# Optimization experiments

Hardware: AMD Instinct MI355X
Metric: run time of the kernel (lower is better)

## Reference

```python
import jax, jax.numpy as jnp
import numpy as np

N = 40000          # nodes
E = 640000         # edges
D_IN, D_HID, D_EMB, D_OUT = 128, 128, 64, 2


def glorot(key, shape):
    lim = np.sqrt(6.0 / (shape[0] + shape[1]))
    return jax.random.uniform(key, shape, jnp.float32, -lim, lim)


def setup_inputs() -> dict:
    key = jax.random.key(0)
    ks = jax.random.split(key, 8)
    x = jax.random.normal(ks[0], (N, D_IN), jnp.float32)
    edge_index = jax.random.randint(ks[1], (2, E), 0, N, dtype=jnp.int64)
    # GCNConv weights stored as [in, out]; biases zero-init per PyG default
    W1 = glorot(ks[2], (D_IN, D_HID));  b1 = jnp.zeros((D_HID,), jnp.float32)
    W2 = glorot(ks[3], (D_HID, D_HID)); b2 = jnp.zeros((D_HID,), jnp.float32)
    W3 = glorot(ks[4], (D_HID, D_EMB)); b3 = jnp.zeros((D_EMB,), jnp.float32)
    Wout = glorot(ks[5], (D_EMB, D_OUT)); bout = jnp.zeros((D_OUT,), jnp.float32)
    return {"x": x, "edge_index": edge_index,
            "W1": W1, "b1": b1, "W2": W2, "b2": b2,
            "W3": W3, "b3": b3, "Wout": Wout, "bout": bout}


def _gcn_norm(edge_index, n):
    # add self loops, compute symmetric normalization d^-1/2[src] * d^-1/2[dst]
    loop = jnp.arange(n, dtype=edge_index.dtype)
    src = jnp.concatenate([edge_index[0], loop])
    dst = jnp.concatenate([edge_index[1], loop])
    deg = jax.ops.segment_sum(jnp.ones_like(dst, dtype=jnp.float32), dst,
                              num_segments=n)
    dinv = jax.lax.rsqrt(deg)                      # deg >= 1 due to self-loops
    dinv = jnp.where(jnp.isinf(dinv), 0.0, dinv)
    return src, dst, dinv[src] * dinv[dst]


def gcn_conv(x, src, dst, norm, W, b):
    h = x @ W                                      # [N, out]
    msg = h[src] * norm[:, None]                   # gather + scale  [E+N, out]
    return jax.ops.segment_sum(msg, dst, num_segments=x.shape[0]) + b


def reference(x, edge_index, W1, b1, W2, b2, W3, b3, Wout, bout):
    n = x.shape[0]
    src, dst, norm = _gcn_norm(edge_index, n)      # cached=True: computed once
    h = jax.nn.relu(gcn_conv(x, src, dst, norm, W1, b1))   # dropout is identity in eval
    h = jax.nn.relu(gcn_conv(h, src, dst, norm, W2, b2))
    h = gcn_conv(h, src, dst, norm, W3, b3)
    out = h @ Wout + bout
    return (out, h)
```

## Files before the change

kernel.cpp:

```cpp
#include <hip/hip_runtime.h>
#include <hip/hip_bf16.h>

#define NN 40000
#define NE 640000

typedef unsigned int u32;
typedef unsigned short u16;
typedef __attribute__((ext_vector_type(8))) short bf16x8;
typedef __attribute__((ext_vector_type(4))) float f32x4;

__device__ float g_wf[512];
__device__ u16   g_wp[40960];
__device__ int   g_flags[4];
__device__ int   g_cnt[NN];
__device__ int   g_cur[NN];
__device__ int   g_rowptr[NN + 1];
__device__ float g_dinv[NN];
__device__ int   g_csrc[NE];
__device__ int   g_bsum[64];
__device__ u16   g_ha[(size_t)NN * 128];
__device__ u16   g_hb[(size_t)NN * 128];

#define OFF_B1 0
#define OFF_B2 128
#define OFF_B3 256
#define OFF_WO 320
#define OFF_BO 448
#define WP_W1 0
#define WP_W2 16384
#define WP_W3 32768

__device__ __forceinline__ float b2f(u16 v){ return __uint_as_float(((u32)v) << 16); }
__device__ __forceinline__ float blo(u32 u){ return __uint_as_float(u << 16); }
__device__ __forceinline__ float bhi(u32 u){ return __uint_as_float(u & 0xffff0000u); }
__device__ __forceinline__ u32 f2bf(float f){
  u32 u = __float_as_uint(f);
  return (u + 0x7fffu + ((u >> 16) & 1u)) >> 16;
}
__device__ __forceinline__ int clampi(int v, int lo, int hi){ return v < lo ? lo : (v > hi ? hi : v); }
__device__ __forceinline__ u16 ldbf(const void* p, int idx){
  return g_flags[0] ? (u16)f2bf(((const float*)p)[idx]) : ((const u16*)p)[idx];
}
__device__ __forceinline__ float ldf(const void* p, int idx){
  return g_flags[0] ? ((const float*)p)[idx] : b2f(((const u16*)p)[idx]);
}

__global__ __launch_bounds__(256) void k_detect(const u16* __restrict__ xf, const int* __restrict__ ei){
  __shared__ int c1, c2;
  if (threadIdx.x == 0){ c1 = 0; c2 = 0; }
  __syncthreads();
  int l1 = 0, l2 = 0;
  for (int i = threadIdx.x; i < 4096; i += 256){
    u16 v = xf[2 * i];
    int e = (v >> 7) & 0xff;
    if (v == 0 || (e >= 100 && e <= 140)) l1++;
    if (ei[2 * i + 1] == 0) l2++;
  }
  atomicAdd(&c1, l1); atomicAdd(&c2, l2);
  __syncthreads();
  if (threadIdx.x == 0){
    g_flags[0] = (c1 < 2048) ? 1 : 0;
    g_flags[1] = (c2 > 2048) ? 2 : 1;
  }
}

__global__ __launch_bounds__(256) void k_prep(const void* xin, const void* w1, const void* b1,
                                              const void* w2, const void* b2, const void* w3,
                                              const void* b3, const void* wo, const void* bo){
  int T = (int)blockIdx.x * 256 + (int)threadIdx.x;
  if (T < 640000){
    if (g_flags[0]){
      const float4* p = (const float4*)xin + (size_t)T * 2;
      float4 a = p[0], b = p[1];
      uint4 o;
      o.x = f2bf(a.x) | (f2bf(a.y) << 16);
      o.y = f2bf(a.z) | (f2bf(a.w) << 16);
      o.z = f2bf(b.x) | (f2bf(b.y) << 16);
      o.w = f2bf(b.z) | (f2bf(b.w) << 16);
      ((uint4*)g_ha)[T] = o;
    } else {
      ((uint4*)g_ha)[T] = ((const uint4*)xin)[T];
    }
  } else if (T < 680960){
    int local = T - 640000;
    int J, dstbase, l; const void* src;
    if (local < 16384){ J = 128; src = w1; dstbase = WP_W1; l = local; }
    else if (local < 32768){ J = 128; src = w2; dstbase = WP_W2; l = local - 16384; }
    else { J = 64; src = w3; dstbase = WP_W3; l = local - 32768; }
    int chunk = l >> 9, within = l & 511;
    int nbw = J / 16;
    int kb = chunk / nbw, nb = chunk % nbw;
    int lane = within >> 3, j = within & 7;
    int q = lane >> 4, n = lane & 15;
    int k = kb * 32 + q * 8 + j;
    int col = nb * 16 + n;
    g_wp[dstbase + l] = ldbf(src, k * J + col);
  } else if (T < 681410){
    int l = T - 680960;
    if (l < 128)      g_wf[OFF_B1 + l] = ldf(b1, l);
    else if (l < 256) g_wf[OFF_B2 + l - 128] = ldf(b2, l - 128);
    else if (l < 320) g_wf[OFF_B3 + l - 256] = ldf(b3, l - 256);
    else if (l < 448) g_wf[OFF_WO + l - 320] = ldf(wo, l - 320);
    else              g_wf[OFF_BO + l - 448] = ldf(bo, l - 448);
  } else if (T < 721410){
    g_cnt[T - 681410] = 0;
  } else if (T < 761450){
    g_cur[T - 721410] = 0;
  }
}

__global__ __launch_bounds__(256) void k_count(const int* __restrict__ ei){
  int e = blockIdx.x * 256 + threadIdx.x;
  if (e < NE){
    int strd = g_flags[1];
    int d = clampi(ei[(size_t)(NE + e) * strd], 0, NN - 1);
    atomicAdd(&g_cnt[d], 1);
  }
}

__global__ __launch_bounds__(1024) void k_scan1(){
  int t = (int)threadIdx.x;
  int b = (int)blockIdx.x;
  int i = b * 1024 + t;
  int v = (i < NN) ? g_cnt[i] : 0;
  int lane = t & 63, wv = t >> 6;
  int x = v;
#pragma unroll
  for (int ofs = 1; ofs < 64; ofs <<= 1){
    int y = __shfl_up(x, ofs, 64);
    if (lane >= ofs) x += y;
  }
  __shared__ int wsum[16];
  if (lane == 63) wsum[wv] = x;
  __syncthreads();
  if (t < 16){
    int s = wsum[t];
#pragma unroll
    for (int ofs = 1; ofs < 16; ofs <<= 1){
      int y = __shfl_up(s, ofs, 64);
      if (t >= ofs) s += y;
    }
    wsum[t] = s;
  }
  __syncthreads();
  int pre = (wv == 0) ? 0 : wsum[wv - 1];
  int incl = x + pre;
  if (i < NN){
    g_rowptr[i] = incl - v;
    g_dinv[i] = rsqrtf((float)(v + 1));
  }
  if (t == 1023) g_bsum[b] = incl;
}

__global__ __launch_bounds__(1024) void k_scan3(){
  __shared__ int pre;
  int t = (int)threadIdx.x;
  if (t < 64){
    int v = (t < 40) ? g_bsum[t] : 0;
    int s = v;
#pragma unroll
    for (int ofs = 1; ofs < 64; ofs <<= 1){
      int y = __shfl_up(s, ofs, 64);
      if (t >= ofs) s += y;
    }
    if (t == (int)blockIdx.x) pre = s - v;
    if (blockIdx.x == 0 && t == 39) g_rowptr[NN] = s;
  }
  __syncthreads();
  int i = (int)blockIdx.x * 1024 + t;
  if (i < NN) g_rowptr[i] += pre;
}

__global__ __launch_bounds__(256) void k_fill(const int* __restrict__ ei){
  int part = (int)blockIdx.x & 7;
  int chunk = (int)blockIdx.x >> 3;
  int lo = part * 5000, hi = lo + 5000;
  int strd = g_flags[1];
  int tid = (int)threadIdx.x;
#pragma unroll
  for (int it = 0; it < 8; ++it){
    int e = chunk * 2048 + it * 256 + tid;
    if (e < NE){
      int d = clampi(ei[(size_t)(NE + e) * strd], 0, NN - 1);
      if (d >= lo && d < hi){
        int s = clampi(ei[(size_t)e * strd], 0, NN - 1);
        int pos = clampi(g_rowptr[d] + atomicAdd(&g_cur[d], 1), 0, NE - 1);
        g_csrc[pos] = s;
      }
    }
  }
}

template<int J>
__global__ __launch_bounds__(256) void k_gemm(int wpoff){
  constexpr int NB = J / 16;
  int tid = (int)threadIdx.x;
  int wave = tid >> 6, lane = tid & 63;
  int q = lane >> 4, n = lane & 15;
  int m0 = (int)blockIdx.x * 64 + wave * 16;
  f32x4 acc[NB];
#pragma unroll
  for (int nb = 0; nb < NB; ++nb) acc[nb] = (f32x4){0.f, 0.f, 0.f, 0.f};
  const u16* arow = g_ha + (size_t)(m0 + n) * 128 + q * 8;
#pragma unroll
  for (int kb = 0; kb < 4; ++kb){
    bf16x8 a = *(const bf16x8*)(arow + kb * 32);
    const u16* wbase = g_wp + wpoff + (kb * NB) * 512 + lane * 8;
#pragma unroll
    for (int nb = 0; nb < NB; ++nb){
      bf16x8 w = *(const bf16x8*)(wbase + nb * 512);
      acc[nb] = __builtin_amdgcn_mfma_f32_16x16x32_bf16(a, w, acc[nb], 0, 0, 0);
    }
  }
  u16* crow = g_hb + (size_t)(m0 + q * 4) * J + n;
#pragma unroll
  for (int r = 0; r < 4; ++r){
    float di = g_dinv[m0 + q * 4 + r];
#pragma unroll
    for (int nb = 0; nb < NB; ++nb)
      crow[(size_t)r * J + nb * 16] = (u16)f2bf(acc[nb][r] * di);
  }
}

template<int J, bool RELU>
__global__ __launch_bounds__(256) void k_agg(int boff, float* __restrict__ h3, float* __restrict__ outp){
  int wpair = (int)((blockIdx.x * 256 + threadIdx.x) >> 6);
  int lane = (int)threadIdx.x & 63;
  int sub = lane >> 5, sl = lane & 31;
  int wid = wpair * 2 + sub;
  if (wid >= NN) return;
  float di = g_dinv[wid];
  int beg = g_rowptr[wid], end = g_rowptr[wid + 1];
  if (J == 128){
    int cc = sl * 4;
    float a0 = 0.f, a1 = 0.f, a2 = 0.f, a3 = 0.f;
    int e = beg;
    for (; e + 7 < end; e += 8){
      int s[8]; uint2 p[8];
#pragma unroll
      for (int t = 0; t < 8; ++t) s[t] = clampi(g_csrc[e + t], 0, NN - 1);
#pragma unroll
      for (int t = 0; t < 8; ++t) p[t] = *(const uint2*)(g_hb + (size_t)s[t] * 128 + cc);
#pragma unroll
      for (int t = 0; t < 8; ++t){
        a0 += blo(p[t].x); a1 += bhi(p[t].x);
        a2 += blo(p[t].y); a3 += bhi(p[t].y);
      }
    }
    for (; e < end; ++e){
      int s0 = clampi(g_csrc[e], 0, NN - 1);
      uint2 p0 = *(const uint2*)(g_hb + (size_t)s0 * 128 + cc);
      a0 += blo(p0.x); a1 += bhi(p0.x);
      a2 += blo(p0.y); a3 += bhi(p0.y);
    }
    uint2 ps = *(const uint2*)(g_hb + (size_t)wid * 128 + cc);
    a0 += blo(ps.x); a1 += bhi(ps.x);
    a2 += blo(ps.y); a3 += bhi(ps.y);
    a0 = a0 * di + g_wf[boff + cc];
    a1 = a1 * di + g_wf[boff + cc + 1];
    a2 = a2 * di + g_wf[boff + cc + 2];
    a3 = a3 * di + g_wf[boff + cc + 3];
    if (RELU){
      a0 = fmaxf(a0, 0.f); a1 = fmaxf(a1, 0.f);
      a2 = fmaxf(a2, 0.f); a3 = fmaxf(a3, 0.f);
    }
    uint2 o;
    o.x = f2bf(a0) | (f2bf(a1) << 16);
    o.y = f2bf(a2) | (f2bf(a3) << 16);
    *(uint2*)(g_ha + (size_t)wid * 128 + cc) = o;
  } else {
    int cc = sl * 2;
    float a0 = 0.f, a1 = 0.f;
    int e = beg;
    for (; e + 7 < end; e += 8){
      int s[8]; u32 p[8];
#pragma unroll
      for (int t = 0; t < 8; ++t) s[t] = clampi(g_csrc[e + t], 0, NN - 1);
#pragma unroll
      for (int t = 0; t < 8; ++t) p[t] = *(const u32*)(g_hb + (size_t)s[t] * 64 + cc);
#pragma unroll
      for (int t = 0; t < 8; ++t){ a0 += blo(p[t]); a1 += bhi(p[t]); }
    }
    for (; e < end; ++e){
      int s0 = clampi(g_csrc[e], 0, NN - 1);
      u32 p0 = *(const u32*)(g_hb + (size_t)s0 * 64 + cc);
      a0 += blo(p0); a1 += bhi(p0);
    }
    u32 ps = *(const u32*)(g_hb + (size_t)wid * 64 + cc);
    a0 += blo(ps); a1 += bhi(ps);
    a0 = a0 * di + g_wf[boff + cc];
    a1 = a1 * di + g_wf[boff + cc + 1];
    if (RELU){ a0 = fmaxf(a0, 0.f); a1 = fmaxf(a1, 0.f); }
    *(float2*)(h3 + (size_t)wid * 64 + cc) = make_float2(a0, a1);
    float o0 = a0 * g_wf[OFF_WO + cc * 2]     + a1 * g_wf[OFF_WO + cc * 2 + 2];
    float o1 = a0 * g_wf[OFF_WO + cc * 2 + 1] + a1 * g_wf[OFF_WO + cc * 2 + 3];
#pragma unroll
    for (int m = 1; m < 32; m <<= 1){
      o0 += __shfl_xor(o0, m, 64);
      o1 += __shfl_xor(o1, m, 64);
    }
    if (sl == 0){
      *(float2*)(outp + (size_t)wid * 2) =
        make_float2(o0 + g_wf[OFF_BO], o1 + g_wf[OFF_BO + 1]);
    }
  }
}

extern "C" void kernel_launch(void* const* d_in, const int* in_sizes, int n_in,
                              void* d_out, int out_size, void* d_ws, size_t ws_size,
                              hipStream_t stream){
  const int* ei = (const int*)d_in[1];
  float* out = (float*)d_out;
  float* h3  = out + (size_t)NN * 2;

  k_detect<<<1, 256, 0, stream>>>((const u16*)d_in[0], ei);
  k_prep<<<2975, 256, 0, stream>>>(d_in[0], d_in[2], d_in[3], d_in[4], d_in[5],
                                   d_in[6], d_in[7], d_in[8], d_in[9]);
  k_count<<<2500, 256, 0, stream>>>(ei);
  k_scan1<<<40, 1024, 0, stream>>>();
  k_scan3<<<40, 1024, 0, stream>>>();
  k_fill<<<2504, 256, 0, stream>>>(ei);

  k_gemm<128><<<625, 256, 0, stream>>>(WP_W1);
  k_agg<128, true><<<5000, 256, 0, stream>>>(OFF_B1, (float*)nullptr, (float*)nullptr);
  k_gemm<128><<<625, 256, 0, stream>>>(WP_W2);
  k_agg<128, true><<<5000, 256, 0, stream>>>(OFF_B2, (float*)nullptr, (float*)nullptr);
  k_gemm<64><<<625, 256, 0, stream>>>(WP_W3);
  k_agg<64, false><<<5000, 256, 0, stream>>>(OFF_B3, h3, out);
}
```

Measured before the change: 259.9 us.

## Compact edge indices to 16-bit and simplify CSR fill to one pass

The count kernel now also writes source and destination indices as 16-bit values into compact arrays. The fill kernel reads these instead of re-scanning the strided int64 edge list with an 8-way partitioned pass, and writes a 16-bit CSR column array. The aggregation kernels then read half the index bytes and skip the clamps. Node ids below 65536 fit in u16, but the fill loses its partition-by-destination locality, which may increase atomic contention.

```diff
diff --git a/kernel.cpp b/kernel.cpp
--- a/kernel.cpp
+++ b/kernel.cpp
@@ -16,7 +16,9 @@
 __device__ int   g_cur[NN];
 __device__ int   g_rowptr[NN + 1];
 __device__ float g_dinv[NN];
-__device__ int   g_csrc[NE];
+__device__ u16   g_es[NE];
+__device__ u16   g_ed[NE];
+__device__ u16   g_csrc16[NE];
 __device__ int   g_bsum[64];
 __device__ u16   g_ha[(size_t)NN * 128];
 __device__ u16   g_hb[(size_t)NN * 128];
@@ -113,7 +115,10 @@
   int e = blockIdx.x * 256 + threadIdx.x;
   if (e < NE){
     int strd = g_flags[1];
+    int s = clampi(ei[(size_t)e * strd], 0, NN - 1);
     int d = clampi(ei[(size_t)(NE + e) * strd], 0, NN - 1);
+    g_es[e] = (u16)s;
+    g_ed[e] = (u16)d;
     atomicAdd(&g_cnt[d], 1);
   }
 }
@@ -171,23 +176,12 @@
   if (i < NN) g_rowptr[i] += pre;
 }
 
-__global__ __launch_bounds__(256) void k_fill(const int* __restrict__ ei){
-  int part = (int)blockIdx.x & 7;
-  int chunk = (int)blockIdx.x >> 3;
-  int lo = part * 5000, hi = lo + 5000;
-  int strd = g_flags[1];
-  int tid = (int)threadIdx.x;
-#pragma unroll
-  for (int it = 0; it < 8; ++it){
-    int e = chunk * 2048 + it * 256 + tid;
-    if (e < NE){
-      int d = clampi(ei[(size_t)(NE + e) * strd], 0, NN - 1);
-      if (d >= lo && d < hi){
-        int s = clampi(ei[(size_t)e * strd], 0, NN - 1);
-        int pos = clampi(g_rowptr[d] + atomicAdd(&g_cur[d], 1), 0, NE - 1);
-        g_csrc[pos] = s;
-      }
-    }
+__global__ __launch_bounds__(256) void k_fill(){
+  int e = blockIdx.x * 256 + threadIdx.x;
+  if (e < NE){
+    int d = g_ed[e];
+    int pos = clampi(g_rowptr[d] + atomicAdd(&g_cur[d], 1), 0, NE - 1);
+    g_csrc16[pos] = g_es[e];
   }
 }
 
@@ -238,7 +232,7 @@
     for (; e + 7 < end; e += 8){
       int s[8]; uint2 p[8];
 #pragma unroll
-      for (int t = 0; t < 8; ++t) s[t] = clampi(g_csrc[e + t], 0, NN - 1);
+      for (int t = 0; t < 8; ++t) s[t] = g_csrc16[e + t];
 #pragma unroll
       for (int t = 0; t < 8; ++t) p[t] = *(const uint2*)(g_hb + (size_t)s[t] * 128 + cc);
 #pragma unroll
@@ -248,7 +242,7 @@
       }
     }
     for (; e < end; ++e){
-      int s0 = clampi(g_csrc[e], 0, NN - 1);
+      int s0 = g_csrc16[e];
       uint2 p0 = *(const uint2*)(g_hb + (size_t)s0 * 128 + cc);
       a0 += blo(p0.x); a1 += bhi(p0.x);
       a2 += blo(p0.y); a3 += bhi(p0.y);
@@ -275,14 +269,14 @@
     for (; e + 7 < end; e += 8){
       int s[8]; u32 p[8];
 #pragma unroll
-      for (int t = 0; t < 8; ++t) s[t] = clampi(g_csrc[e + t], 0, NN - 1);
+      for (int t = 0; t < 8; ++t) s[t] = g_csrc16[e + t];
 #pragma unroll
       for (int t = 0; t < 8; ++t) p[t] = *(const u32*)(g_hb + (size_t)s[t] * 64 + cc);
 #pragma unroll
       for (int t = 0; t < 8; ++t){ a0 += blo(p[t]); a1 += bhi(p[t]); }
     }
     for (; e < end; ++e){
-      int s0 = clampi(g_csrc[e], 0, NN - 1);
+      int s0 = g_csrc16[e];
       u32 p0 = *(const u32*)(g_hb + (size_t)s0 * 64 + cc);
       a0 += blo(p0); a1 += bhi(p0);
     }
@@ -319,7 +313,7 @@
   k_count<<<2500, 256, 0, stream>>>(ei);
   k_scan1<<<40, 1024, 0, stream>>>();
   k_scan3<<<40, 1024, 0, stream>>>();
-  k_fill<<<2504, 256, 0, stream>>>(ei);
+  k_fill<<<2500, 256, 0, stream>>>();
 
   k_gemm<128><<<625, 256, 0, stream>>>(WP_W1);
   k_agg<128, true><<<5000, 256, 0, stream>>>(OFF_B1, (float*)nullptr, (float*)nullptr);
```

Result: slower. 274.9 us (+5.8%).
